# Performance work log

Hardware: AMD Instinct MI355X
Metric: run time of the kernel (lower is better)

Reference implementation:

```python
import jax, jax.numpy as jnp
import numpy as np

NUM_HEADS = 16
ROPE_BASE = 10000.0


def _apply_rope(x, cos, sin):
    # x: [B, S, Hh, Dh]; cos/sin: [1, S, 1, Dh//2]; NeoX style (rotate halves)
    half = x.shape[-1] // 2
    x1, x2 = x[..., :half], x[..., half:]
    return jnp.concatenate([x1 * cos - x2 * sin, x2 * cos + x1 * sin], axis=-1)


def setup_inputs() -> dict:
    key = jax.random.key(0)
    ks = jax.random.split(key, 5)
    B, S, H = 4, 2048, 1024
    std = 1.0 / np.sqrt(H)
    return {
        "positions": jnp.arange(S, dtype=jnp.int32),
        "hidden_states": jax.random.normal(ks[0], (B, S, H), dtype=jnp.float32),
        "Wqkv": jax.random.normal(ks[1], (H, 3 * H), dtype=jnp.float32) * std,
        "bqkv": jax.random.normal(ks[2], (3 * H,), dtype=jnp.float32) * 0.02,
        "Wout": jax.random.normal(ks[3], (H, H), dtype=jnp.float32) * std,
        "bout": jax.random.normal(ks[4], (H,), dtype=jnp.float32) * 0.02,
    }


def reference(positions, hidden_states, Wqkv, bqkv, Wout, bout):
    B, S, H = hidden_states.shape
    Hh = NUM_HEADS
    Dh = H // Hh
    scale = Dh ** -0.5

    # fused QKV projection
    qkv = hidden_states @ Wqkv + bqkv                      # [B, S, 3H]
    q, k, v = jnp.split(qkv, 3, axis=-1)
    q = q.reshape(B, S, Hh, Dh)
    k = k.reshape(B, S, Hh, Dh)
    v = v.reshape(B, S, Hh, Dh)

    # NeoX-style RoPE over full head_dim
    half = Dh // 2
    inv_freq = 1.0 / (ROPE_BASE ** (jnp.arange(half, dtype=jnp.float32) / half))
    freqs = positions.astype(jnp.float32)[:, None] * inv_freq  # [S, half]
    cos = jnp.cos(freqs)[None, :, None, :]
    sin = jnp.sin(freqs)[None, :, None, :]
    q = _apply_rope(q, cos, sin)
    k = _apply_rope(k, cos, sin)

    # encoder-only (bidirectional) SDPA
    scores = jnp.einsum("bqhd,bkhd->bhqk", q, k) * scale   # [B, Hh, S, S]
    attn = jax.nn.softmax(scores, axis=-1)
    ctx = jnp.einsum("bhqk,bkhd->bqhd", attn, v).reshape(B, S, H)

    # output projection
    return ctx @ Wout + bout
```

## Files before the change

### kernel.cpp

```cpp
#include <hip/hip_runtime.h>
#include <hip/hip_bf16.h>

namespace {

constexpr int Bsz = 4, S = 2048, H = 1024, HH = 16, DH = 64;
constexpr int M = Bsz * S;
constexpr int NQKV = 3 * H;
constexpr float SCALE = 0.125f;
constexpr float NEG_LOG_BASE_OVER_HALF = -0.2878231366242557f;

typedef float f32x4 __attribute__((ext_vector_type(4)));
typedef short short8_t __attribute__((ext_vector_type(8)));
typedef short short4_t __attribute__((ext_vector_type(4)));

__device__ __forceinline__ void glds16(const void* g, void* l) {
  __builtin_amdgcn_global_load_lds(
      (const __attribute__((address_space(1))) void*)g,
      (__attribute__((address_space(3))) void*)l, 16, 0, 0);
}

__device__ __forceinline__ short f2bf(float f) {
  __hip_bfloat16 h = __float2bfloat16(f);
  return *reinterpret_cast<short*>(&h);
}

__global__ void cvt_f32_bf16(const float* __restrict__ src, short* __restrict__ dst, int n4) {
  int i = blockIdx.x * blockDim.x + threadIdx.x;
  const int stride = gridDim.x * blockDim.x;
  const float4* s4 = reinterpret_cast<const float4*>(src);
  short4_t* d4 = reinterpret_cast<short4_t*>(dst);
  for (; i < n4; i += stride) {
    float4 f = s4[i];
    short4_t o;
    o.x = f2bf(f.x); o.y = f2bf(f.y); o.z = f2bf(f.z); o.w = f2bf(f.w);
    d4[i] = o;
  }
}

__global__ void tconv(const float* __restrict__ src, short* __restrict__ dst, int R, int C) {
  __shared__ float t[32][33];
  const int c0 = blockIdx.x * 32, r0 = blockIdx.y * 32;
  for (int i = threadIdx.y; i < 32; i += 8)
    t[i][threadIdx.x] = src[(r0 + i) * C + c0 + threadIdx.x];
  __syncthreads();
  for (int i = threadIdx.y; i < 32; i += 8)
    dst[(c0 + i) * R + r0 + threadIdx.x] = f2bf(t[threadIdx.x][i]);
}

__global__ void rope_tab(const int* __restrict__ positions, float* __restrict__ ctab,
                         float* __restrict__ stab) {
  const int i = blockIdx.x * blockDim.x + threadIdx.x;
  const int s = i >> 5, d = i & 31;
  const float ang = (float)positions[s] * expf((float)d * NEG_LOG_BASE_OVER_HALF);
  ctab[i] = cosf(ang);
  stab[i] = sinf(ang);
}

__global__ __launch_bounds__(256, 2)
void gemm_qkv(const short* __restrict__ X, const short* __restrict__ Wt,
              const float* __restrict__ bias, const float* __restrict__ ctab,
              const float* __restrict__ stab,
              short* __restrict__ Qo, short* __restrict__ Ko, short* __restrict__ Vo) {
  __shared__ __align__(16) short As[128 * 32];
  __shared__ __align__(16) short Bs[128 * 32];
  const int tid = threadIdx.x, lane = tid & 63, wid = tid >> 6;
  const int l15 = lane & 15, hi = lane >> 4;
  const int m0 = blockIdx.x * 128, n0 = blockIdx.y * 128;
  const int wr = wid >> 1, wc = wid & 1;
  f32x4 acc[4][4];
#pragma unroll
  for (int m = 0; m < 4; ++m)
#pragma unroll
    for (int n = 0; n < 4; ++n) acc[m][n] = (f32x4){0.f, 0.f, 0.f, 0.f};

  for (int kt = 0; kt < 32; ++kt) {
    const int k0 = kt * 32;
    __syncthreads();
#pragma unroll
    for (int j = 0; j < 2; ++j) {
      const int c = j * 256 + wid * 64 + lane;
      glds16(X + (m0 + (c >> 2)) * 1024 + k0 + (c & 3) * 8,
             (char*)As + (j * 256 + wid * 64) * 16);
      glds16(Wt + (n0 + (c >> 2)) * 1024 + k0 + (c & 3) * 8,
             (char*)Bs + (j * 256 + wid * 64) * 16);
    }
    __syncthreads();
    short8_t a[4], b[4];
#pragma unroll
    for (int m = 0; m < 4; ++m)
      a[m] = *(const short8_t*)&As[(wr * 64 + m * 16 + l15) * 32 + hi * 8];
#pragma unroll
    for (int n = 0; n < 4; ++n)
      b[n] = *(const short8_t*)&Bs[(wc * 64 + n * 16 + l15) * 32 + hi * 8];
#pragma unroll
    for (int m = 0; m < 4; ++m)
#pragma unroll
      for (int n = 0; n < 4; ++n)
        acc[m][n] = __builtin_amdgcn_mfma_f32_16x16x32_bf16(a[m], b[n], acc[m][n], 0, 0, 0);
  }

  const int colbase = n0 + wc * 64;
  const int sec = colbase >> 10;
  const int hh = (colbase & 1023) >> 6;
  if (sec == 2) {
#pragma unroll
    for (int m = 0; m < 4; ++m)
#pragma unroll
      for (int r = 0; r < 4; ++r) {
        const int grow = m0 + wr * 64 + m * 16 + hi * 4 + r;
        const int b = grow >> 11, s = grow & 2047;
#pragma unroll
        for (int n = 0; n < 4; ++n) {
          const int d = n * 16 + l15;
          Vo[((b * HH + hh) * DH + d) * S + s] = f2bf(acc[m][n][r] + bias[colbase + d]);
        }
      }
  } else {
    short* const outp = (sec == 0) ? Qo : Ko;
#pragma unroll
    for (int m = 0; m < 4; ++m)
#pragma unroll
      for (int r = 0; r < 4; ++r) {
        const int grow = m0 + wr * 64 + m * 16 + hi * 4 + r;
        const int b = grow >> 11, s = grow & 2047;
        const int base = ((b * HH + hh) * S + s) * DH;
#pragma unroll
        for (int n = 0; n < 2; ++n) {
          const int d1 = n * 16 + l15;
          const float x1 = acc[m][n][r] + bias[colbase + d1];
          const float x2 = acc[m][n + 2][r] + bias[colbase + d1 + 32];
          const float cs = ctab[s * 32 + d1], sn = stab[s * 32 + d1];
          outp[base + d1] = f2bf(x1 * cs - x2 * sn);
          outp[base + d1 + 32] = f2bf(x2 * cs + x1 * sn);
        }
      }
  }
}

__global__ __launch_bounds__(256, 2)
void attn(const short* __restrict__ Q, const short* __restrict__ K,
          const short* __restrict__ Vt, short* __restrict__ ctx) {
  __shared__ __align__(16) short Kl[64 * 64];
  __shared__ __align__(16) short Vl[64 * 64];
  __shared__ __align__(16) short Pf[4 * 1024];
  const int tid = threadIdx.x, lane = tid & 63, wid = tid >> 6;
  const int l15 = lane & 15, hi = lane >> 4;
  const int bh = blockIdx.y;
  const int q0 = blockIdx.x * 64;
  const short* Qb = Q + bh * (S * DH);
  const short* Kb = K + bh * (S * DH);
  const short* Vb = Vt + bh * (DH * S);

  const int qrow = q0 + wid * 16 + l15;
  short8_t qf[2];
  qf[0] = *(const short8_t*)&Qb[qrow * 64 + hi * 8];
  qf[1] = *(const short8_t*)&Qb[qrow * 64 + 32 + hi * 8];

  const int sigl = (lane >> 2) + (lane & 3) * 16;

  f32x4 o[4];
  float mrun[4], lrun[4];
#pragma unroll
  for (int i = 0; i < 4; ++i) { o[i] = (f32x4){0.f, 0.f, 0.f, 0.f}; mrun[i] = -1e30f; lrun[i] = 0.f; }

  for (int kt = 0; kt < 32; ++kt) {
    __syncthreads();
#pragma unroll
    for (int j = 0; j < 2; ++j) {
      const int c = j * 256 + wid * 64 + lane;
      const int row = c >> 3;
      const int swz = ((c & 7) * 16) ^ ((row & 7) << 4);
      glds16((const char*)(Kb + (kt * 64 + row) * 64) + swz,
             (char*)Kl + (j * 256 + wid * 64) * 16);
    }
#pragma unroll
    for (int j = 0; j < 2; ++j) {
      const int c = j * 256 + tid;
      const int row = c >> 3;
      const int q = (c & 7) ^ (row & 7);
      short8_t vv = *(const short8_t*)&Vb[row * S + kt * 64 + q * 8];
      *(short8_t*)&Vl[row * 64 + (c & 7) * 8] = vv;
    }
    __syncthreads();

    f32x4 s4[4];
#pragma unroll
    for (int nf = 0; nf < 4; ++nf) {
      s4[nf] = (f32x4){0.f, 0.f, 0.f, 0.f};
      const int scol = nf * 16 + l15;
#pragma unroll
      for (int st = 0; st < 2; ++st) {
        short8_t kf = *(const short8_t*)((const char*)Kl + scol * 128 +
                                         ((st * 64 + hi * 16) ^ ((scol & 7) << 4)));
        s4[nf] = __builtin_amdgcn_mfma_f32_16x16x32_bf16(qf[st], kf, s4[nf], 0, 0, 0);
      }
    }

    float fr[4];
#pragma unroll
    for (int r = 0; r < 4; ++r) {
      float mx = fmaxf(fmaxf(s4[0][r], s4[1][r]), fmaxf(s4[2][r], s4[3][r]));
#pragma unroll
      for (int msk = 1; msk < 16; msk <<= 1) mx = fmaxf(mx, __shfl_xor(mx, msk, 64));
      const float mnew = fmaxf(mrun[r], mx * SCALE);
      fr[r] = __expf(mrun[r] - mnew);
      float rs = 0.f;
#pragma unroll
      for (int nf = 0; nf < 4; ++nf) {
        const float p = __expf(s4[nf][r] * SCALE - mnew);
        s4[nf][r] = p;
        rs += p;
      }
#pragma unroll
      for (int msk = 1; msk < 16; msk <<= 1) rs += __shfl_xor(rs, msk, 64);
      lrun[r] = lrun[r] * fr[r] + rs;
      mrun[r] = mnew;
    }
#pragma unroll
    for (int nf = 0; nf < 4; ++nf)
#pragma unroll
      for (int r = 0; r < 4; ++r) o[nf][r] *= fr[r];

#pragma unroll
    for (int nf = 0; nf < 4; ++nf)
#pragma unroll
      for (int r = 0; r < 4; ++r) {
        const int k = nf * 16 + l15;
        const int st = k >> 5, kk = k & 31;
        const int ROW = (kk >> 3) * 16 + hi * 4 + r;
        const int sig = (ROW >> 2) + (ROW & 3) * 16;
        Pf[wid * 1024 + st * 512 + sig * 8 + (kk & 7)] = f2bf(s4[nf][r]);
      }
    asm volatile("s_waitcnt lgkmcnt(0)" ::: "memory");
    short8_t pa0 = *(const short8_t*)&Pf[wid * 1024 + sigl * 8];
    short8_t pa1 = *(const short8_t*)&Pf[wid * 1024 + 512 + sigl * 8];

#pragma unroll
    for (int nf = 0; nf < 4; ++nf) {
      const int d = nf * 16 + l15;
#pragma unroll
      for (int st = 0; st < 2; ++st) {
        short8_t vf = *(const short8_t*)((const char*)Vl + d * 128 +
                                         ((st * 64 + hi * 16) ^ ((d & 7) << 4)));
        o[nf] = __builtin_amdgcn_mfma_f32_16x16x32_bf16(st == 0 ? pa0 : pa1, vf, o[nf], 0, 0, 0);
      }
    }
  }

  const int b = bh >> 4, h = bh & 15;
#pragma unroll
  for (int nf = 0; nf < 4; ++nf)
#pragma unroll
    for (int r = 0; r < 4; ++r) {
      const int s = q0 + wid * 16 + hi * 4 + r;
      ctx[(b * S + s) * H + h * 64 + nf * 16 + l15] = f2bf(o[nf][r] / lrun[r]);
    }
}

__global__ __launch_bounds__(256, 2)
void gemm_out(const short* __restrict__ A, const short* __restrict__ Wt,
              const float* __restrict__ bias, float* __restrict__ out) {
  __shared__ __align__(16) short As[128 * 32];
  __shared__ __align__(16) short Bs[128 * 32];
  const int tid = threadIdx.x, lane = tid & 63, wid = tid >> 6;
  const int l15 = lane & 15, hi = lane >> 4;
  const int m0 = blockIdx.x * 128, n0 = blockIdx.y * 128;
  const int wr = wid >> 1, wc = wid & 1;
  f32x4 acc[4][4];
#pragma unroll
  for (int m = 0; m < 4; ++m)
#pragma unroll
    for (int n = 0; n < 4; ++n) acc[m][n] = (f32x4){0.f, 0.f, 0.f, 0.f};

  for (int kt = 0; kt < 32; ++kt) {
    const int k0 = kt * 32;
    __syncthreads();
#pragma unroll
    for (int j = 0; j < 2; ++j) {
      const int c = j * 256 + wid * 64 + lane;
      glds16(A + (m0 + (c >> 2)) * 1024 + k0 + (c & 3) * 8,
             (char*)As + (j * 256 + wid * 64) * 16);
      glds16(Wt + (n0 + (c >> 2)) * 1024 + k0 + (c & 3) * 8,
             (char*)Bs + (j * 256 + wid * 64) * 16);
    }
    __syncthreads();
    short8_t a[4], b[4];
#pragma unroll
    for (int m = 0; m < 4; ++m)
      a[m] = *(const short8_t*)&As[(wr * 64 + m * 16 + l15) * 32 + hi * 8];
#pragma unroll
    for (int n = 0; n < 4; ++n)
      b[n] = *(const short8_t*)&Bs[(wc * 64 + n * 16 + l15) * 32 + hi * 8];
#pragma unroll
    for (int m = 0; m < 4; ++m)
#pragma unroll
      for (int n = 0; n < 4; ++n)
        acc[m][n] = __builtin_amdgcn_mfma_f32_16x16x32_bf16(a[m], b[n], acc[m][n], 0, 0, 0);
  }

#pragma unroll
  for (int m = 0; m < 4; ++m)
#pragma unroll
    for (int r = 0; r < 4; ++r) {
      const int grow = m0 + wr * 64 + m * 16 + hi * 4 + r;
#pragma unroll
      for (int n = 0; n < 4; ++n) {
        const int gcol = n0 + wc * 64 + n * 16 + l15;
        out[grow * 1024 + gcol] = acc[m][n][r] + bias[gcol];
      }
    }
}

}

extern "C" void kernel_launch(void* const* d_in, const int* in_sizes, int n_in,
                              void* d_out, int out_size, void* d_ws, size_t ws_size,
                              hipStream_t stream) {
  const int* positions = (const int*)d_in[0];
  const float* hidden = (const float*)d_in[1];
  const float* Wqkv = (const float*)d_in[2];
  const float* bqkv = (const float*)d_in[3];
  const float* Wout = (const float*)d_in[4];
  const float* bout = (const float*)d_in[5];
  float* out = (float*)d_out;
  char* ws = (char*)d_ws;

  short* Xb  = (short*)(ws + 0);
  short* Wb  = (short*)(ws + 16777216);
  short* Wob = (short*)(ws + 23068672);
  short* Qb  = (short*)(ws + 25165824);
  short* Kb  = (short*)(ws + 41943040);
  short* Vtb = (short*)(ws + 58720256);
  float* ctab = (float*)(ws + 75497472);
  float* stab = (float*)(ws + 75759616);
  short* Cb  = Xb;

  cvt_f32_bf16<<<1024, 256, 0, stream>>>(hidden, Xb, (Bsz * S * H) / 4);
  tconv<<<dim3(NQKV / 32, H / 32), dim3(32, 8), 0, stream>>>(Wqkv, Wb, H, NQKV);
  tconv<<<dim3(H / 32, H / 32), dim3(32, 8), 0, stream>>>(Wout, Wob, H, H);
  rope_tab<<<(S * 32) / 256, 256, 0, stream>>>(positions, ctab, stab);
  gemm_qkv<<<dim3(M / 128, NQKV / 128), 256, 0, stream>>>(Xb, Wb, bqkv, ctab, stab, Qb, Kb, Vtb);
  attn<<<dim3(S / 64, Bsz * HH), 256, 0, stream>>>(Qb, Kb, Vtb, Cb);
  gemm_out<<<dim3(M / 128, H / 128), 256, 0, stream>>>(Cb, Wob, bout, out);
}
```

Baseline: 404.1 us.

## Rewrite attention with 32x32 MFMA, transposed S, register P exchange

Switches the flash-attention kernel from 16x16x32 to 32x32x16 MFMA and computes S transposed (K as A operand), so each lane owns one query row. Row max and sum need only a single cross-half shuffle, and P is repacked to bf16 through lane shuffles instead of a round trip through LDS. Each block now handles 128 queries (32 per wave) instead of 64, which halves the K/V tile reloads per query. The softmax scale is folded into Q in the QKV GEMM epilogue. Register pressure rises and the grid has half as many blocks.

```diff
diff --git a/kernel.cpp b/kernel.cpp
--- a/kernel.cpp
+++ b/kernel.cpp
@@ -6,12 +6,14 @@
 constexpr int Bsz = 4, S = 2048, H = 1024, HH = 16, DH = 64;
 constexpr int M = Bsz * S;
 constexpr int NQKV = 3 * H;
-constexpr float SCALE = 0.125f;
 constexpr float NEG_LOG_BASE_OVER_HALF = -0.2878231366242557f;
 
 typedef float f32x4 __attribute__((ext_vector_type(4)));
+typedef float f32x16 __attribute__((ext_vector_type(16)));
 typedef short short8_t __attribute__((ext_vector_type(8)));
 typedef short short4_t __attribute__((ext_vector_type(4)));
+
+union U32x4S8 { uint4 u; short8_t s; };
 
 __device__ __forceinline__ void glds16(const void* g, void* l) {
   __builtin_amdgcn_global_load_lds(
@@ -117,6 +119,7 @@
       }
   } else {
     short* const outp = (sec == 0) ? Qo : Ko;
+    const float qsc = (sec == 0) ? 0.125f : 1.0f;
 #pragma unroll
     for (int m = 0; m < 4; ++m)
 #pragma unroll
@@ -130,8 +133,8 @@
           const float x1 = acc[m][n][r] + bias[colbase + d1];
           const float x2 = acc[m][n + 2][r] + bias[colbase + d1 + 32];
           const float cs = ctab[s * 32 + d1], sn = stab[s * 32 + d1];
-          outp[base + d1] = f2bf(x1 * cs - x2 * sn);
-          outp[base + d1 + 32] = f2bf(x2 * cs + x1 * sn);
+          outp[base + d1] = f2bf((x1 * cs - x2 * sn) * qsc);
+          outp[base + d1 + 32] = f2bf((x2 * cs + x1 * sn) * qsc);
         }
       }
   }
@@ -142,26 +145,24 @@
           const short* __restrict__ Vt, short* __restrict__ ctx) {
   __shared__ __align__(16) short Kl[64 * 64];
   __shared__ __align__(16) short Vl[64 * 64];
-  __shared__ __align__(16) short Pf[4 * 1024];
   const int tid = threadIdx.x, lane = tid & 63, wid = tid >> 6;
-  const int l15 = lane & 15, hi = lane >> 4;
+  const int col = lane & 31, h = lane >> 5;
   const int bh = blockIdx.y;
-  const int q0 = blockIdx.x * 64;
+  const int q0 = blockIdx.x * 128;
   const short* Qb = Q + bh * (S * DH);
   const short* Kb = K + bh * (S * DH);
   const short* Vb = Vt + bh * (DH * S);
 
-  const int qrow = q0 + wid * 16 + l15;
-  short8_t qf[2];
-  qf[0] = *(const short8_t*)&Qb[qrow * 64 + hi * 8];
-  qf[1] = *(const short8_t*)&Qb[qrow * 64 + 32 + hi * 8];
-
-  const int sigl = (lane >> 2) + (lane & 3) * 16;
-
-  f32x4 o[4];
-  float mrun[4], lrun[4];
-#pragma unroll
-  for (int i = 0; i < 4; ++i) { o[i] = (f32x4){0.f, 0.f, 0.f, 0.f}; mrun[i] = -1e30f; lrun[i] = 0.f; }
+  const int qrow = q0 + wid * 32 + col;
+  short8_t qf[4];
+#pragma unroll
+  for (int st = 0; st < 4; ++st)
+    qf[st] = *(const short8_t*)&Qb[qrow * 64 + st * 16 + h * 8];
+
+  f32x16 o0, o1;
+#pragma unroll
+  for (int r = 0; r < 16; ++r) { o0[r] = 0.f; o1[r] = 0.f; }
+  float mrun = -1e30f, lrun = 0.f;
 
   for (int kt = 0; kt < 32; ++kt) {
     __syncthreads();
@@ -183,78 +184,68 @@
     }
     __syncthreads();
 
-    f32x4 s4[4];
-#pragma unroll
-    for (int nf = 0; nf < 4; ++nf) {
-      s4[nf] = (f32x4){0.f, 0.f, 0.f, 0.f};
-      const int scol = nf * 16 + l15;
-#pragma unroll
-      for (int st = 0; st < 2; ++st) {
-        short8_t kf = *(const short8_t*)((const char*)Kl + scol * 128 +
-                                         ((st * 64 + hi * 16) ^ ((scol & 7) << 4)));
-        s4[nf] = __builtin_amdgcn_mfma_f32_16x16x32_bf16(qf[st], kf, s4[nf], 0, 0, 0);
-      }
-    }
-
-    float fr[4];
-#pragma unroll
-    for (int r = 0; r < 4; ++r) {
-      float mx = fmaxf(fmaxf(s4[0][r], s4[1][r]), fmaxf(s4[2][r], s4[3][r]));
-#pragma unroll
-      for (int msk = 1; msk < 16; msk <<= 1) mx = fmaxf(mx, __shfl_xor(mx, msk, 64));
-      const float mnew = fmaxf(mrun[r], mx * SCALE);
-      fr[r] = __expf(mrun[r] - mnew);
+#pragma unroll
+    for (int sub = 0; sub < 2; ++sub) {
+      const int kv = sub * 32 + col;
+      f32x16 s;
+#pragma unroll
+      for (int r = 0; r < 16; ++r) s[r] = 0.f;
+#pragma unroll
+      for (int dstep = 0; dstep < 4; ++dstep) {
+        short8_t af = *(const short8_t*)((const char*)Kl + kv * 128 +
+                                         ((dstep * 32 + h * 16) ^ ((kv & 7) << 4)));
+        s = __builtin_amdgcn_mfma_f32_32x32x16_bf16(af, qf[dstep], s, 0, 0, 0);
+      }
+      float smax = s[0];
+#pragma unroll
+      for (int r = 1; r < 16; ++r) smax = fmaxf(smax, s[r]);
+      smax = fmaxf(smax, __shfl_xor(smax, 32, 64));
+      const float mnew = fmaxf(mrun, smax);
+      const float fr = __expf(mrun - mnew);
+      float p[16];
       float rs = 0.f;
 #pragma unroll
-      for (int nf = 0; nf < 4; ++nf) {
-        const float p = __expf(s4[nf][r] * SCALE - mnew);
-        s4[nf][r] = p;
-        rs += p;
-      }
-#pragma unroll
-      for (int msk = 1; msk < 16; msk <<= 1) rs += __shfl_xor(rs, msk, 64);
-      lrun[r] = lrun[r] * fr[r] + rs;
-      mrun[r] = mnew;
-    }
-#pragma unroll
-    for (int nf = 0; nf < 4; ++nf)
-#pragma unroll
-      for (int r = 0; r < 4; ++r) o[nf][r] *= fr[r];
-
-#pragma unroll
-    for (int nf = 0; nf < 4; ++nf)
-#pragma unroll
-      for (int r = 0; r < 4; ++r) {
-        const int k = nf * 16 + l15;
-        const int st = k >> 5, kk = k & 31;
-        const int ROW = (kk >> 3) * 16 + hi * 4 + r;
-        const int sig = (ROW >> 2) + (ROW & 3) * 16;
-        Pf[wid * 1024 + st * 512 + sig * 8 + (kk & 7)] = f2bf(s4[nf][r]);
-      }
-    asm volatile("s_waitcnt lgkmcnt(0)" ::: "memory");
-    short8_t pa0 = *(const short8_t*)&Pf[wid * 1024 + sigl * 8];
-    short8_t pa1 = *(const short8_t*)&Pf[wid * 1024 + 512 + sigl * 8];
-
-#pragma unroll
-    for (int nf = 0; nf < 4; ++nf) {
-      const int d = nf * 16 + l15;
-#pragma unroll
-      for (int st = 0; st < 2; ++st) {
-        short8_t vf = *(const short8_t*)((const char*)Vl + d * 128 +
-                                         ((st * 64 + hi * 16) ^ ((d & 7) << 4)));
-        o[nf] = __builtin_amdgcn_mfma_f32_16x16x32_bf16(st == 0 ? pa0 : pa1, vf, o[nf], 0, 0, 0);
-      }
-    }
-  }
-
-  const int b = bh >> 4, h = bh & 15;
-#pragma unroll
-  for (int nf = 0; nf < 4; ++nf)
-#pragma unroll
-    for (int r = 0; r < 4; ++r) {
-      const int s = q0 + wid * 16 + hi * 4 + r;
-      ctx[(b * S + s) * H + h * 64 + nf * 16 + l15] = f2bf(o[nf][r] / lrun[r]);
-    }
+      for (int r = 0; r < 16; ++r) { p[r] = __expf(s[r] - mnew); rs += p[r]; }
+      rs += __shfl_xor(rs, 32, 64);
+      lrun = lrun * fr + rs;
+      mrun = mnew;
+#pragma unroll
+      for (int r = 0; r < 16; ++r) { o0[r] *= fr; o1[r] *= fr; }
+
+      uint w[8], sw[8];
+#pragma unroll
+      for (int j = 0; j < 8; ++j)
+        w[j] = (uint)(ushort)f2bf(p[2 * j]) | ((uint)(ushort)f2bf(p[2 * j + 1]) << 16);
+#pragma unroll
+      for (int j = 0; j < 8; ++j)
+        sw[j] = (uint)__shfl_xor((int)w[j], 32, 64);
+      U32x4S8 b0, b1;
+      b0.u.x = h ? sw[2] : w[0];  b0.u.y = h ? sw[3] : w[1];
+      b0.u.z = h ? w[2] : sw[0];  b0.u.w = h ? w[3] : sw[1];
+      b1.u.x = h ? sw[6] : w[4];  b1.u.y = h ? sw[7] : w[5];
+      b1.u.z = h ? w[6] : sw[4];  b1.u.w = h ? w[7] : sw[5];
+
+#pragma unroll
+      for (int st2 = 0; st2 < 2; ++st2) {
+        const short8_t pb = st2 ? b1.s : b0.s;
+        const int cb = (sub * 64 + st2 * 32 + h * 16) ^ ((col & 7) << 4);
+        short8_t vf0 = *(const short8_t*)((const char*)Vl + col * 128 + cb);
+        o0 = __builtin_amdgcn_mfma_f32_32x32x16_bf16(vf0, pb, o0, 0, 0, 0);
+        short8_t vf1 = *(const short8_t*)((const char*)Vl + (32 + col) * 128 + cb);
+        o1 = __builtin_amdgcn_mfma_f32_32x32x16_bf16(vf1, pb, o1, 0, 0, 0);
+      }
+    }
+  }
+
+  const float inv = 1.0f / lrun;
+  const int b = bh >> 4, hh = bh & 15;
+  const long obase = (long)(b * S + qrow) * H + hh * 64;
+#pragma unroll
+  for (int r = 0; r < 16; ++r) {
+    const int d = (r & 3) + 8 * (r >> 2) + 4 * h;
+    ctx[obase + d] = f2bf(o0[r] * inv);
+    ctx[obase + 32 + d] = f2bf(o1[r] * inv);
+  }
 }
 
 __global__ __launch_bounds__(256, 2)
@@ -340,6 +331,6 @@
   tconv<<<dim3(H / 32, H / 32), dim3(32, 8), 0, stream>>>(Wout, Wob, H, H);
   rope_tab<<<(S * 32) / 256, 256, 0, stream>>>(positions, ctab, stab);
   gemm_qkv<<<dim3(M / 128, NQKV / 128), 256, 0, stream>>>(Xb, Wb, bqkv, ctab, stab, Qb, Kb, Vtb);
-  attn<<<dim3(S / 64, Bsz * HH), 256, 0, stream>>>(Qb, Kb, Vtb, Cb);
+  attn<<<dim3(S / 128, Bsz * HH), 256, 0, stream>>>(Qb, Kb, Vtb, Cb);
   gemm_out<<<dim3(M / 128, H / 128), 256, 0, stream>>>(Cb, Wob, bout, out);
 }
```

Result: faster. 323.7 us (-19.9%).
